# Kernel optimization log

Measured on AMD Instinct MI355X. Metric: run time of the kernel, lower is better.

Reference implementation:

```python
import jax, jax.numpy as jnp
import numpy as np

N, E, IN_F, G, LATENT, HIDDEN, STEPS = 50000, 800000, 7, 16, 64, 128, 3
LN_EPS = 1e-6  # flax LayerNorm default


def setup_inputs() -> dict:
    key = jax.random.key(0)

    def rn(i, shape, scale=1.0):
        return jax.random.normal(jax.random.fold_in(key, i), shape, dtype=jnp.float32) * scale

    return {
        "nodes": rn(0, (N, IN_F)),
        "senders": jax.random.randint(jax.random.fold_in(key, 1), (E,), 0, N, dtype=jnp.int32),
        "receivers": jax.random.randint(jax.random.fold_in(key, 2), (E,), 0, N, dtype=jnp.int32),
        "g": rn(3, (G,)),
        "embed_w": rn(4, (IN_F, LATENT), IN_F ** -0.5),
        "embed_b": jnp.zeros((LATENT,), jnp.float32),
        "edge_w1_first": rn(5, (2 * LATENT + G, HIDDEN), (2 * LATENT + G) ** -0.5),
        "edge_w1_rest": rn(6, (STEPS - 1, 3 * LATENT + G, HIDDEN), (3 * LATENT + G) ** -0.5),
        "edge_b1": jnp.zeros((STEPS, HIDDEN), jnp.float32),
        "edge_w2": rn(7, (STEPS, HIDDEN, LATENT), HIDDEN ** -0.5),
        "edge_b2": jnp.zeros((STEPS, LATENT), jnp.float32),
        "node_w1": rn(8, (STEPS, 2 * LATENT + G, HIDDEN), (2 * LATENT + G) ** -0.5),
        "node_b1": jnp.zeros((STEPS, HIDDEN), jnp.float32),
        "node_w2": rn(9, (STEPS, HIDDEN, LATENT), HIDDEN ** -0.5),
        "node_b2": jnp.zeros((STEPS, LATENT), jnp.float32),
        "ln_scale": jnp.ones((STEPS, LATENT), jnp.float32),
        "ln_bias": jnp.zeros((STEPS, LATENT), jnp.float32),
        "dec_w": rn(10, (LATENT, IN_F), LATENT ** -0.5),
        "dec_b": jnp.zeros((IN_F,), jnp.float32),
    }


def _layer_norm(x, scale, bias):
    mu = jnp.mean(x, axis=-1, keepdims=True)
    var = jnp.var(x, axis=-1, keepdims=True)
    return (x - mu) * jax.lax.rsqrt(var + LN_EPS) * scale + bias


def reference(nodes, senders, receivers, g, embed_w, embed_b,
              edge_w1_first, edge_w1_rest, edge_b1, edge_w2, edge_b2,
              node_w1, node_b1, node_w2, node_b2, ln_scale, ln_bias,
              dec_w, dec_b):
    n_node = nodes.shape[0]
    n_edge = senders.shape[0]
    # node embedder (GraphMapFeatures with Dense(latent_size))
    h = nodes @ embed_w + embed_b                      # [N, LATENT]
    ge = jnp.broadcast_to(g[None, :], (n_edge, g.shape[0]))  # globals per edge
    gn = jnp.broadcast_to(g[None, :], (n_node, g.shape[0]))  # globals per node
    e = None
    for t in range(STEPS):
        s = h[senders]                                 # [E, LATENT] gather
        r = h[receivers]                               # [E, LATENT] gather
        if t == 0:
            # edges are None on the first step -> concat(senders, receivers, globals)
            e_in = jnp.concatenate([s, r, ge], axis=1)
            w1 = edge_w1_first
        else:
            e_in = jnp.concatenate([e, s, r, ge], axis=1)
            w1 = edge_w1_rest[t - 1]
        # edge MLP: Dense(hidden)+gelu, Dense(latent)
        e = jax.nn.gelu(e_in @ w1 + edge_b1[t]) @ edge_w2[t] + edge_b2[t]
        # aggregate messages at receivers (jraph default segment_sum)
        recv = jax.ops.segment_sum(e, receivers, num_segments=n_node)
        # node MLP on concat(nodes, received, globals)
        n_in = jnp.concatenate([h, recv, gn], axis=1)
        upd = jax.nn.gelu(n_in @ node_w1[t] + node_b1[t]) @ node_w2[t] + node_b2[t]
        h = h + upd                                    # skip connection on nodes
        h = _layer_norm(h, ln_scale[t], ln_bias[t])
    # node decoder back to in_features
    return h @ dec_w + dec_b
```

## Files before the change

### kernel.cpp

```cpp
#include <hip/hip_runtime.h>

#define NN 50000
#define NE 800000
#define INF 7
#define GD 16
#define LAT 64
#define HID 128

typedef unsigned short u16;
typedef __attribute__((ext_vector_type(8))) __bf16 bf16x8;
typedef __attribute__((ext_vector_type(4))) float f32x4;

__device__ __forceinline__ float bf2f(u16 u) {
  union { unsigned int i; float f; } v; v.i = ((unsigned int)u) << 16; return v.f;
}
__device__ __forceinline__ u16 f2bf(float f) {
  union { float f; unsigned int i; } v; v.f = f;
  unsigned int x = v.i;
  return (u16)((x + 0x7fffu + ((x >> 16) & 1u)) >> 16);
}
__device__ __forceinline__ float gelu(float x) {
  float u = x * x;
  float p = fmaf(0.044715f * u, x, x);
  float e = __expf(-1.5957691216057308f * p);
  return x * __builtin_amdgcn_rcpf(e + 1.0f);
}

struct PackJobs {
  const float* src[13];
  u16* dst[13];
  int K[13];
  int N[13];
  int KC[13];
};

__global__ void pack_all(PackJobs J) {
  const int j = blockIdx.y;
  const int KC = J.KC[j];
  const float* W = J.src[j];
  u16* out = J.dst[j];
  int t = blockIdx.x * blockDim.x + threadIdx.x;
  if (KC == 0) {
    if (t < 32) out[t] = (t < GD) ? f2bf(W[t]) : (u16)0;
    return;
  }
  const int K = J.K[j], N = J.N[j];
  const int NT = N >> 4;
  if (t >= KC * NT * 64) return;
  int l = t & 63;
  int nt = (t >> 6) % NT;
  int kc = t / (64 * NT);
  int n = nt * 16 + (l & 15);
  int kbase = kc * 32 + (l >> 4) * 8;
  ushort4 lo, hi;
  u16 v[8];
#pragma unroll
  for (int jj = 0; jj < 8; ++jj) {
    int k = kbase + jj;
    v[jj] = (k < K) ? f2bf(W[k * N + n]) : (u16)0;
  }
  lo.x = v[0]; lo.y = v[1]; lo.z = v[2]; lo.w = v[3];
  hi.x = v[4]; hi.y = v[5]; hi.z = v[6]; hi.w = v[7];
  ushort4* dst = (ushort4*)&out[(size_t)t * 8];
  dst[0] = lo; dst[1] = hi;
}

__global__ void embed_kernel(const float* __restrict__ nodes, const float* __restrict__ w,
                             const float* __restrict__ b, float* __restrict__ h,
                             u16* __restrict__ hbf) {
  int gid = blockIdx.x * blockDim.x + threadIdx.x;
  if (gid >= NN * LAT) return;
  int n = gid >> 6, j = gid & 63;
  float acc = b[j];
#pragma unroll
  for (int k = 0; k < INF; ++k)
    acc = fmaf(nodes[n * INF + k], w[k * LAT + j], acc);
  h[gid] = acc;
  hbf[gid] = f2bf(acc);
}

template <int KC, bool FIRST>
__launch_bounds__(256)
__global__ void edge_mfma(const u16* __restrict__ hbf, u16* __restrict__ ebuf,
                          float* __restrict__ recvbuf,
                          const int* __restrict__ snd, const int* __restrict__ rcv,
                          const u16* __restrict__ gpad,
                          const u16* __restrict__ w1p, const float* __restrict__ b1,
                          const u16* __restrict__ w2p, const float* __restrict__ b2) {
  __shared__ __align__(16) u16 hid[32 * 136];
  __shared__ __align__(16) u16 easm[32 * 64];
  __shared__ int rcvs[32];

  const int tid = threadIdx.x;
  const int lane = tid & 63;
  const int w = tid >> 6;
  const int l15 = lane & 15;
  const int q = lane >> 4;
  const int mr = w & 1;
  const int ntb1 = (w >> 1) * 4;
  const int ntb2 = (w >> 1) * 2;
  const int arow = mr * 16 + l15;
  const int NTILE = NE / 32;

  float bb1[4], bb2[2];
#pragma unroll
  for (int i = 0; i < 4; ++i) bb1[i] = b1[(ntb1 + i) * 16 + l15];
#pragma unroll
  for (int i = 0; i < 2; ++i) bb2[i] = b2[(ntb2 + i) * 16 + l15];

  int s_cur = 0, r_cur = 0;
  if (blockIdx.x < NTILE) {
    const int eg0 = blockIdx.x * 32 + arow;
    s_cur = snd[eg0];
    r_cur = rcv[eg0];
  }

  for (int tile = blockIdx.x; tile < NTILE; tile += gridDim.x) {
    const int ebase = tile * 32;
    const int eg = ebase + arow;
    const int soff = s_cur * 64;
    const int roff = r_cur * 64;
    if (tid < 32) rcvs[tid] = rcv[ebase + tid];

    {
      int tn = tile + gridDim.x;
      if (tn < NTILE) {
        const int egn = tn * 32 + arow;
        s_cur = snd[egn];
        r_cur = rcv[egn];
      }
    }

    {
      f32x4 acc[4];
#pragma unroll
      for (int i = 0; i < 4; ++i) acc[i] = (f32x4){bb1[i], bb1[i], bb1[i], bb1[i]};
#pragma unroll
      for (int kc = 0; kc < KC; ++kc) {
        const u16* abase;
        if (FIRST) {
          abase = (kc < 2) ? &hbf[soff + kc * 32]
                : (kc < 4) ? &hbf[roff + (kc - 2) * 32]
                :            &gpad[0];
        } else {
          abase = (kc < 2) ? &ebuf[(size_t)eg * 64 + kc * 32]
                : (kc < 4) ? &hbf[soff + (kc - 2) * 32]
                : (kc < 6) ? &hbf[roff + (kc - 4) * 32]
                :            &gpad[0];
        }
        bf16x8 a = *(const bf16x8*)&abase[q * 8];
#pragma unroll
        for (int i = 0; i < 4; ++i) {
          bf16x8 b = *(const bf16x8*)&w1p[(size_t)((kc * 8 + ntb1 + i) * 64 + lane) * 8];
          acc[i] = __builtin_amdgcn_mfma_f32_16x16x32_bf16(a, b, acc[i], 0, 0, 0);
        }
      }
#pragma unroll
      for (int i = 0; i < 4; ++i) {
        const int col = (ntb1 + i) * 16 + l15;
#pragma unroll
        for (int r4 = 0; r4 < 4; ++r4) {
          const int row = mr * 16 + q * 4 + r4;
          hid[row * 136 + col] = f2bf(gelu(acc[i][r4]));
        }
      }
    }
    __syncthreads();
    {
      f32x4 acc[2];
#pragma unroll
      for (int i = 0; i < 2; ++i) acc[i] = (f32x4){bb2[i], bb2[i], bb2[i], bb2[i]};
#pragma unroll
      for (int kc = 0; kc < 4; ++kc) {
        bf16x8 a = *(const bf16x8*)&hid[arow * 136 + kc * 32 + q * 8];
#pragma unroll
        for (int i = 0; i < 2; ++i) {
          bf16x8 b = *(const bf16x8*)&w2p[(size_t)((kc * 4 + ntb2 + i) * 64 + lane) * 8];
          acc[i] = __builtin_amdgcn_mfma_f32_16x16x32_bf16(a, b, acc[i], 0, 0, 0);
        }
      }
#pragma unroll
      for (int i = 0; i < 2; ++i) {
        const int col = (ntb2 + i) * 16 + l15;
#pragma unroll
        for (int r4 = 0; r4 < 4; ++r4) {
          const int row = mr * 16 + q * 4 + r4;
          const float v = acc[i][r4];
          easm[row * 64 + col] = f2bf(v);
          atomicAdd(&recvbuf[(size_t)rcvs[row] * 64 + col], v);
        }
      }
    }
    __syncthreads();
    ((uint4*)&ebuf[(size_t)ebase * 64])[tid] = ((const uint4*)easm)[tid];
  }
}

__launch_bounds__(256)
__global__ void node_mfma(float* __restrict__ h, u16* __restrict__ hbf,
                          const float* __restrict__ recvb,
                          const u16* __restrict__ gpad,
                          const u16* __restrict__ w1p, const float* __restrict__ b1,
                          const u16* __restrict__ w2p, const float* __restrict__ b2,
                          const float* __restrict__ lns, const float* __restrict__ lnb) {
  __shared__ __align__(16) u16 hid[32 * 136];
  __shared__ __align__(16) float outs[32 * 68];

  const int tid = threadIdx.x;
  const int lane = tid & 63;
  const int w = tid >> 6;
  const int l15 = lane & 15;
  const int q = lane >> 4;
  const int mr = w & 1;
  const int ntb1 = (w >> 1) * 4;
  const int ntb2 = (w >> 1) * 2;
  const int arow = mr * 16 + l15;

  float bb1[4], bb2[2];
#pragma unroll
  for (int i = 0; i < 4; ++i) bb1[i] = b1[(ntb1 + i) * 16 + l15];
#pragma unroll
  for (int i = 0; i < 2; ++i) bb2[i] = b2[(ntb2 + i) * 16 + l15];

  const int nrow = tid >> 3;
  const int jc = (tid & 7) * 8;
  float sc8[8], bi8[8];
#pragma unroll
  for (int k = 0; k < 8; ++k) { sc8[k] = lns[jc + k]; bi8[k] = lnb[jc + k]; }

  const int NT = (NN + 31) / 32;
  for (int tile = blockIdx.x; tile < NT; tile += gridDim.x) {
    const int nbase = tile * 32;
    const int na = min(nbase + arow, NN - 1) * 64;

    {
      f32x4 acc[4];
#pragma unroll
      for (int i = 0; i < 4; ++i) acc[i] = (f32x4){bb1[i], bb1[i], bb1[i], bb1[i]};
#pragma unroll
      for (int kc = 0; kc < 5; ++kc) {
        bf16x8 a;
        if (kc < 2) {
          a = *(const bf16x8*)&hbf[na + kc * 32 + q * 8];
        } else if (kc < 4) {
          const float* rp = &recvb[na + (kc - 2) * 32 + q * 8];
          union { u16 u[8]; bf16x8 v; } cv;
#pragma unroll
          for (int jj = 0; jj < 8; ++jj) cv.u[jj] = f2bf(rp[jj]);
          a = cv.v;
        } else {
          a = *(const bf16x8*)&gpad[q * 8];
        }
#pragma unroll
        for (int i = 0; i < 4; ++i) {
          bf16x8 b = *(const bf16x8*)&w1p[(size_t)((kc * 8 + ntb1 + i) * 64 + lane) * 8];
          acc[i] = __builtin_amdgcn_mfma_f32_16x16x32_bf16(a, b, acc[i], 0, 0, 0);
        }
      }
#pragma unroll
      for (int i = 0; i < 4; ++i) {
        const int col = (ntb1 + i) * 16 + l15;
#pragma unroll
        for (int r4 = 0; r4 < 4; ++r4) {
          const int row = mr * 16 + q * 4 + r4;
          hid[row * 136 + col] = f2bf(gelu(acc[i][r4]));
        }
      }
    }
    __syncthreads();
    {
      f32x4 acc[2];
#pragma unroll
      for (int i = 0; i < 2; ++i) acc[i] = (f32x4){bb2[i], bb2[i], bb2[i], bb2[i]};
#pragma unroll
      for (int kc = 0; kc < 4; ++kc) {
        bf16x8 a = *(const bf16x8*)&hid[arow * 136 + kc * 32 + q * 8];
#pragma unroll
        for (int i = 0; i < 2; ++i) {
          bf16x8 b = *(const bf16x8*)&w2p[(size_t)((kc * 4 + ntb2 + i) * 64 + lane) * 8];
          acc[i] = __builtin_amdgcn_mfma_f32_16x16x32_bf16(a, b, acc[i], 0, 0, 0);
        }
      }
#pragma unroll
      for (int i = 0; i < 2; ++i) {
        const int col = (ntb2 + i) * 16 + l15;
#pragma unroll
        for (int r4 = 0; r4 < 4; ++r4) {
          const int row = mr * 16 + q * 4 + r4;
          outs[row * 68 + col] = acc[i][r4];
        }
      }
    }
    __syncthreads();
    {
      const int n = nbase + nrow;
      if (n < NN) {
        float x[8];
        float4 hv0 = *(const float4*)&h[n * 64 + jc];
        float4 hv1 = *(const float4*)&h[n * 64 + jc + 4];
        x[0] = hv0.x + outs[nrow * 68 + jc + 0];
        x[1] = hv0.y + outs[nrow * 68 + jc + 1];
        x[2] = hv0.z + outs[nrow * 68 + jc + 2];
        x[3] = hv0.w + outs[nrow * 68 + jc + 3];
        x[4] = hv1.x + outs[nrow * 68 + jc + 4];
        x[5] = hv1.y + outs[nrow * 68 + jc + 5];
        x[6] = hv1.z + outs[nrow * 68 + jc + 6];
        x[7] = hv1.w + outs[nrow * 68 + jc + 7];
        float s = 0.f, qq = 0.f;
#pragma unroll
        for (int k = 0; k < 8; ++k) { s += x[k]; qq += x[k] * x[k]; }
#pragma unroll
        for (int off = 1; off < 8; off <<= 1) {
          s += __shfl_xor(s, off);
          qq += __shfl_xor(qq, off);
        }
        float mean = s * (1.0f / 64.0f);
        float var = fmaxf(qq * (1.0f / 64.0f) - mean * mean, 0.0f);
        float rstd = rsqrtf(var + 1e-6f);
        float o[8];
        ushort4 ob0, ob1;
#pragma unroll
        for (int k = 0; k < 8; ++k) o[k] = (x[k] - mean) * rstd * sc8[k] + bi8[k];
        *(float4*)&h[n * 64 + jc]     = make_float4(o[0], o[1], o[2], o[3]);
        *(float4*)&h[n * 64 + jc + 4] = make_float4(o[4], o[5], o[6], o[7]);
        ob0.x = f2bf(o[0]); ob0.y = f2bf(o[1]); ob0.z = f2bf(o[2]); ob0.w = f2bf(o[3]);
        ob1.x = f2bf(o[4]); ob1.y = f2bf(o[5]); ob1.z = f2bf(o[6]); ob1.w = f2bf(o[7]);
        *(ushort4*)&hbf[n * 64 + jc]     = ob0;
        *(ushort4*)&hbf[n * 64 + jc + 4] = ob1;
      }
    }
    __syncthreads();
  }
}

__global__ void decode_kernel(const float* __restrict__ h, const float* __restrict__ w,
                              const float* __restrict__ b, float* __restrict__ out) {
  int gid = blockIdx.x * blockDim.x + threadIdx.x;
  if (gid >= NN * INF) return;
  int n = gid / 7, f = gid % 7;
  float acc = b[f];
#pragma unroll
  for (int k = 0; k < LAT; ++k)
    acc = fmaf(h[n * 64 + k], w[k * 7 + f], acc);
  out[gid] = acc;
}

extern "C" void kernel_launch(void* const* d_in, const int* in_sizes, int n_in,
                              void* d_out, int out_size, void* d_ws, size_t ws_size,
                              hipStream_t stream) {
  const float* nodes = (const float*)d_in[0];
  const int* senders = (const int*)d_in[1];
  const int* recvrs  = (const int*)d_in[2];
  const float* g     = (const float*)d_in[3];
  const float* emb_w = (const float*)d_in[4];
  const float* emb_b = (const float*)d_in[5];
  const float* ew1f  = (const float*)d_in[6];
  const float* ew1r  = (const float*)d_in[7];
  const float* eb1   = (const float*)d_in[8];
  const float* ew2   = (const float*)d_in[9];
  const float* eb2   = (const float*)d_in[10];
  const float* nw1   = (const float*)d_in[11];
  const float* nb1   = (const float*)d_in[12];
  const float* nw2   = (const float*)d_in[13];
  const float* nb2   = (const float*)d_in[14];
  const float* lns   = (const float*)d_in[15];
  const float* lnb   = (const float*)d_in[16];
  const float* dw    = (const float*)d_in[17];
  const float* db    = (const float*)d_in[18];

  char* cur = (char*)d_ws;
  float* h      = (float*)cur;  cur += (size_t)NN * LAT * 4;
  float* recvb  = (float*)cur;  cur += (size_t)NN * LAT * 4;
  u16*   ebuf   = (u16*)cur;    cur += (size_t)NE * LAT * 2;
  u16*   hbf    = (u16*)cur;    cur += (size_t)NN * LAT * 2;
  u16*   ew1p[3]; for (int t = 0; t < 3; ++t) { ew1p[t] = (u16*)cur; cur += 7 * 8 * 64 * 8 * 2; }
  u16*   ew2p[3]; for (int t = 0; t < 3; ++t) { ew2p[t] = (u16*)cur; cur += 4 * 4 * 64 * 8 * 2; }
  u16*   nw1p[3]; for (int t = 0; t < 3; ++t) { nw1p[t] = (u16*)cur; cur += 5 * 8 * 64 * 8 * 2; }
  u16*   nw2p[3]; for (int t = 0; t < 3; ++t) { nw2p[t] = (u16*)cur; cur += 4 * 4 * 64 * 8 * 2; }
  u16*   gpad   = (u16*)cur;    cur += 64;

  PackJobs J;
  J.src[0] = ew1f;                       J.dst[0] = ew1p[0]; J.K[0] = 144; J.N[0] = 128; J.KC[0] = 5;
  J.src[1] = ew1r;                       J.dst[1] = ew1p[1]; J.K[1] = 208; J.N[1] = 128; J.KC[1] = 7;
  J.src[2] = ew1r + (size_t)208 * 128;   J.dst[2] = ew1p[2]; J.K[2] = 208; J.N[2] = 128; J.KC[2] = 7;
  for (int t = 0; t < 3; ++t) {
    J.src[3 + t] = ew2 + (size_t)t * 128 * 64;  J.dst[3 + t] = ew2p[t]; J.K[3 + t] = 128; J.N[3 + t] = 64; J.KC[3 + t] = 4;
    J.src[6 + t] = nw1 + (size_t)t * 144 * 128; J.dst[6 + t] = nw1p[t]; J.K[6 + t] = 144; J.N[6 + t] = 128; J.KC[6 + t] = 5;
    J.src[9 + t] = nw2 + (size_t)t * 128 * 64;  J.dst[9 + t] = nw2p[t]; J.K[9 + t] = 128; J.N[9 + t] = 64; J.KC[9 + t] = 4;
  }
  J.src[12] = g; J.dst[12] = gpad; J.K[12] = 0; J.N[12] = 0; J.KC[12] = 0;
  pack_all<<<dim3(16, 13), 256, 0, stream>>>(J);

  embed_kernel<<<(NN * LAT + 255) / 256, 256, 0, stream>>>(nodes, emb_w, emb_b, h, hbf);

  for (int t = 0; t < 3; ++t) {
    hipMemsetAsync(recvb, 0, (size_t)NN * LAT * 4, stream);
    if (t == 0)
      edge_mfma<5, true><<<2048, 256, 0, stream>>>(hbf, ebuf, recvb,
          senders, recvrs, gpad, ew1p[0], eb1, ew2p[0], eb2);
    else
      edge_mfma<7, false><<<2048, 256, 0, stream>>>(hbf, ebuf, recvb,
          senders, recvrs, gpad, ew1p[t], eb1 + t * 128, ew2p[t], eb2 + t * 64);
    node_mfma<<<1563, 256, 0, stream>>>(h, hbf, recvb, gpad,
        nw1p[t], nb1 + t * 128, nw2p[t], nb2 + t * 64,
        lns + t * 64, lnb + t * 64);
  }

  decode_kernel<<<(NN * INF + 255) / 256, 256, 0, stream>>>(h, dw, db, (float*)d_out);
}
```

Baseline: 752.3 us.

## Replace atomic scatter-add with CSR receiver-sorted segment reduction in node kernel

Edges are sorted by receiver once per call (histogram, single-block scan, atomic scatter) into a CSR layout. The edge kernel then processes edges in sorted order and drops the per-element float atomics into the recv buffer and its memset. The node kernel sums each node's incoming bf16 edge messages directly from ebuf via rowptr and stages them in LDS. The cost is extra preprocessing kernels, including a serial one-block scan, and bf16-sourced summation, with load imbalance across nodes of different degree.

```diff
diff --git a/kernel.cpp b/kernel.cpp
--- a/kernel.cpp
+++ b/kernel.cpp
@@ -13,6 +13,12 @@
 
 __device__ __forceinline__ float bf2f(u16 u) {
   union { unsigned int i; float f; } v; v.i = ((unsigned int)u) << 16; return v.f;
+}
+__device__ __forceinline__ float blo(unsigned int u) {
+  union { unsigned int i; float f; } v; v.i = u << 16; return v.f;
+}
+__device__ __forceinline__ float bhi(unsigned int u) {
+  union { unsigned int i; float f; } v; v.i = u & 0xffff0000u; return v.f;
 }
 __device__ __forceinline__ u16 f2bf(float f) {
   union { float f; unsigned int i; } v; v.f = f;
@@ -65,6 +71,42 @@
   dst[0] = lo; dst[1] = hi;
 }
 
+__global__ void hist_kernel(const int* __restrict__ rcv, int* __restrict__ cnt) {
+  int i = blockIdx.x * blockDim.x + threadIdx.x;
+  if (i < NE) atomicAdd(&cnt[rcv[i]], 1);
+}
+
+__global__ void scan_kernel(const int* __restrict__ cnt, int* __restrict__ rowptr,
+                            int* __restrict__ cursor) {
+  __shared__ int psum[256];
+  const int t = threadIdx.x;
+  const int C = (NN + 255) / 256;
+  const int lo = t * C, hi = min(lo + C, NN);
+  int s = 0;
+  for (int i = lo; i < hi; ++i) s += cnt[i];
+  psum[t] = s;
+  __syncthreads();
+  if (t == 0) {
+    int run = 0;
+    for (int i = 0; i < 256; ++i) { int v = psum[i]; psum[i] = run; run += v; }
+  }
+  __syncthreads();
+  int run = psum[t];
+  for (int i = lo; i < hi; ++i) { rowptr[i] = run; cursor[i] = run; run += cnt[i]; }
+  if (hi == NN) rowptr[NN] = NE;
+}
+
+__global__ void scatter_kernel(const int* __restrict__ snd, const int* __restrict__ rcv,
+                               int* __restrict__ cursor, int* __restrict__ ssnd,
+                               int* __restrict__ srcv) {
+  int i = blockIdx.x * blockDim.x + threadIdx.x;
+  if (i >= NE) return;
+  int r = rcv[i];
+  int p = atomicAdd(&cursor[r], 1);
+  ssnd[p] = snd[i];
+  srcv[p] = r;
+}
+
 __global__ void embed_kernel(const float* __restrict__ nodes, const float* __restrict__ w,
                              const float* __restrict__ b, float* __restrict__ h,
                              u16* __restrict__ hbf) {
@@ -82,14 +124,12 @@
 template <int KC, bool FIRST>
 __launch_bounds__(256)
 __global__ void edge_mfma(const u16* __restrict__ hbf, u16* __restrict__ ebuf,
-                          float* __restrict__ recvbuf,
                           const int* __restrict__ snd, const int* __restrict__ rcv,
                           const u16* __restrict__ gpad,
                           const u16* __restrict__ w1p, const float* __restrict__ b1,
                           const u16* __restrict__ w2p, const float* __restrict__ b2) {
   __shared__ __align__(16) u16 hid[32 * 136];
   __shared__ __align__(16) u16 easm[32 * 64];
-  __shared__ int rcvs[32];
 
   const int tid = threadIdx.x;
   const int lane = tid & 63;
@@ -120,7 +160,6 @@
     const int eg = ebase + arow;
     const int soff = s_cur * 64;
     const int roff = r_cur * 64;
-    if (tid < 32) rcvs[tid] = rcv[ebase + tid];
 
     {
       int tn = tile + gridDim.x;
@@ -185,9 +224,7 @@
 #pragma unroll
         for (int r4 = 0; r4 < 4; ++r4) {
           const int row = mr * 16 + q * 4 + r4;
-          const float v = acc[i][r4];
-          easm[row * 64 + col] = f2bf(v);
-          atomicAdd(&recvbuf[(size_t)rcvs[row] * 64 + col], v);
+          easm[row * 64 + col] = f2bf(acc[i][r4]);
         }
       }
     }
@@ -198,12 +235,13 @@
 
 __launch_bounds__(256)
 __global__ void node_mfma(float* __restrict__ h, u16* __restrict__ hbf,
-                          const float* __restrict__ recvb,
+                          const u16* __restrict__ ebuf, const int* __restrict__ rowptr,
                           const u16* __restrict__ gpad,
                           const u16* __restrict__ w1p, const float* __restrict__ b1,
                           const u16* __restrict__ w2p, const float* __restrict__ b2,
                           const float* __restrict__ lns, const float* __restrict__ lnb) {
   __shared__ __align__(16) u16 hid[32 * 136];
+  __shared__ __align__(16) u16 rlds[32 * 72];
   __shared__ __align__(16) float outs[32 * 68];
 
   const int tid = threadIdx.x;
@@ -234,6 +272,27 @@
     const int na = min(nbase + arow, NN - 1) * 64;
 
     {
+      const int n = nbase + nrow;
+      float a8[8] = {0.f, 0.f, 0.f, 0.f, 0.f, 0.f, 0.f, 0.f};
+      if (n < NN) {
+        const int e0 = rowptr[n], e1 = rowptr[n + 1];
+        for (int e = e0; e < e1; ++e) {
+          uint4 v = *(const uint4*)&ebuf[(size_t)e * 64 + jc];
+          a8[0] += blo(v.x); a8[1] += bhi(v.x);
+          a8[2] += blo(v.y); a8[3] += bhi(v.y);
+          a8[4] += blo(v.z); a8[5] += bhi(v.z);
+          a8[6] += blo(v.w); a8[7] += bhi(v.w);
+        }
+      }
+      ushort4 p0, p1;
+      p0.x = f2bf(a8[0]); p0.y = f2bf(a8[1]); p0.z = f2bf(a8[2]); p0.w = f2bf(a8[3]);
+      p1.x = f2bf(a8[4]); p1.y = f2bf(a8[5]); p1.z = f2bf(a8[6]); p1.w = f2bf(a8[7]);
+      *(ushort4*)&rlds[nrow * 72 + jc] = p0;
+      *(ushort4*)&rlds[nrow * 72 + jc + 4] = p1;
+    }
+    __syncthreads();
+
+    {
       f32x4 acc[4];
 #pragma unroll
       for (int i = 0; i < 4; ++i) acc[i] = (f32x4){bb1[i], bb1[i], bb1[i], bb1[i]};
@@ -243,11 +302,7 @@
         if (kc < 2) {
           a = *(const bf16x8*)&hbf[na + kc * 32 + q * 8];
         } else if (kc < 4) {
-          const float* rp = &recvb[na + (kc - 2) * 32 + q * 8];
-          union { u16 u[8]; bf16x8 v; } cv;
-#pragma unroll
-          for (int jj = 0; jj < 8; ++jj) cv.u[jj] = f2bf(rp[jj]);
-          a = cv.v;
+          a = *(const bf16x8*)&rlds[arow * 72 + (kc - 2) * 32 + q * 8];
         } else {
           a = *(const bf16x8*)&gpad[q * 8];
         }
@@ -370,14 +425,23 @@
 
   char* cur = (char*)d_ws;
   float* h      = (float*)cur;  cur += (size_t)NN * LAT * 4;
-  float* recvb  = (float*)cur;  cur += (size_t)NN * LAT * 4;
   u16*   ebuf   = (u16*)cur;    cur += (size_t)NE * LAT * 2;
   u16*   hbf    = (u16*)cur;    cur += (size_t)NN * LAT * 2;
   u16*   ew1p[3]; for (int t = 0; t < 3; ++t) { ew1p[t] = (u16*)cur; cur += 7 * 8 * 64 * 8 * 2; }
   u16*   ew2p[3]; for (int t = 0; t < 3; ++t) { ew2p[t] = (u16*)cur; cur += 4 * 4 * 64 * 8 * 2; }
   u16*   nw1p[3]; for (int t = 0; t < 3; ++t) { nw1p[t] = (u16*)cur; cur += 5 * 8 * 64 * 8 * 2; }
   u16*   nw2p[3]; for (int t = 0; t < 3; ++t) { nw2p[t] = (u16*)cur; cur += 4 * 4 * 64 * 8 * 2; }
-  u16*   gpad   = (u16*)cur;    cur += 64;
+  u16*   gpad   = (u16*)cur;    cur += 256;
+  int*   cnt    = (int*)cur;    cur += ((size_t)NN * 4 + 255) & ~(size_t)255;
+  int*   cursor = (int*)cur;    cur += ((size_t)NN * 4 + 255) & ~(size_t)255;
+  int*   rowptr = (int*)cur;    cur += ((size_t)(NN + 1) * 4 + 255) & ~(size_t)255;
+  int*   ssnd   = (int*)cur;    cur += (size_t)NE * 4;
+  int*   srcv   = (int*)cur;    cur += (size_t)NE * 4;
+
+  hipMemsetAsync(cnt, 0, (size_t)NN * 4, stream);
+  hist_kernel<<<(NE + 255) / 256, 256, 0, stream>>>(recvrs, cnt);
+  scan_kernel<<<1, 256, 0, stream>>>(cnt, rowptr, cursor);
+  scatter_kernel<<<(NE + 255) / 256, 256, 0, stream>>>(senders, recvrs, cursor, ssnd, srcv);
 
   PackJobs J;
   J.src[0] = ew1f;                       J.dst[0] = ew1p[0]; J.K[0] = 144; J.N[0] = 128; J.KC[0] = 5;
@@ -394,14 +458,13 @@
   embed_kernel<<<(NN * LAT + 255) / 256, 256, 0, stream>>>(nodes, emb_w, emb_b, h, hbf);
 
   for (int t = 0; t < 3; ++t) {
-    hipMemsetAsync(recvb, 0, (size_t)NN * LAT * 4, stream);
     if (t == 0)
-      edge_mfma<5, true><<<2048, 256, 0, stream>>>(hbf, ebuf, recvb,
-          senders, recvrs, gpad, ew1p[0], eb1, ew2p[0], eb2);
+      edge_mfma<5, true><<<2048, 256, 0, stream>>>(hbf, ebuf,
+          ssnd, srcv, gpad, ew1p[0], eb1, ew2p[0], eb2);
     else
-      edge_mfma<7, false><<<2048, 256, 0, stream>>>(hbf, ebuf, recvb,
-          senders, recvrs, gpad, ew1p[t], eb1 + t * 128, ew2p[t], eb2 + t * 64);
-    node_mfma<<<1563, 256, 0, stream>>>(h, hbf, recvb, gpad,
+      edge_mfma<7, false><<<2048, 256, 0, stream>>>(hbf, ebuf,
+          ssnd, srcv, gpad, ew1p[t], eb1 + t * 128, ew2p[t], eb2 + t * 64);
+    node_mfma<<<1563, 256, 0, stream>>>(h, hbf, ebuf, rowptr, gpad,
         nw1p[t], nb1 + t * 128, nw2p[t], nb2 + t * 64,
         lns + t * 64, lnb + t * 64);
   }
```

After: 835.2 us. 11.0% more time.
